# Kernel optimization log

Measured on AMD Instinct MI355X. Metric: run time of the kernel, lower is better.

The kernel has to match this reference:

```python
import jax, jax.numpy as jnp
import numpy as np

D_MODEL = 1024
N_HEADS = 16
D_HEAD = D_MODEL // N_HEADS
WINDOW = 256


def setup_inputs() -> dict:
    key = jax.random.key(0)
    ks = jax.random.split(key, 9)
    x = jax.random.normal(ks[0], (1, 4096, D_MODEL), dtype=jnp.float32)
    s = 0.02
    params = {
        'q_w': jax.random.normal(ks[1], (D_MODEL, D_MODEL), jnp.float32) * s,
        'q_b': jax.random.normal(ks[2], (D_MODEL,), jnp.float32) * s,
        'k_w': jax.random.normal(ks[3], (D_MODEL, D_MODEL), jnp.float32) * s,
        'k_b': jax.random.normal(ks[4], (D_MODEL,), jnp.float32) * s,
        'v_w': jax.random.normal(ks[5], (D_MODEL, D_MODEL), jnp.float32) * s,
        'v_b': jax.random.normal(ks[6], (D_MODEL,), jnp.float32) * s,
        'o_w': jax.random.normal(ks[7], (D_MODEL, D_MODEL), jnp.float32) * s,
        'o_b': jax.random.normal(ks[8], (D_MODEL,), jnp.float32) * s,
    }
    return {'x': x, **params}


def reference(x, q_w, q_b, k_w, k_b, v_w, v_b, o_w, o_b):
    B, S, D = x.shape
    scale = jnp.sqrt(jnp.float32(D_HEAD))
    # torch nn.Linear: y = x @ W.T + b
    q = (x @ q_w.T + q_b).reshape(B, S, N_HEADS, D_HEAD).transpose(0, 2, 1, 3)
    k = (x @ k_w.T + k_b).reshape(B, S, N_HEADS, D_HEAD).transpose(0, 2, 1, 3)
    v = (x @ v_w.T + v_b).reshape(B, S, N_HEADS, D_HEAD).transpose(0, 2, 1, 3)
    scores = jnp.einsum('bhqd,bhkd->bhqk', q, k) / scale  # [B,H,S,S]
    idx = jnp.arange(S)
    row = idx[:, None]
    col = idx[None, :]
    masked = (col > row) | (row - col >= min(WINDOW, S))
    scores = jnp.where(masked[None, None], -jnp.inf, scores)
    attn = jax.nn.softmax(scores, axis=-1)
    attn = jnp.nan_to_num(attn, nan=0.0)
    out = jnp.einsum('bhqk,bhkd->bhqd', attn, v)
    out = out.transpose(0, 2, 1, 3).reshape(B, S, D)
    return out @ o_w.T + o_b
```

## Files before the change

### kernel.cpp

```cpp
#include <hip/hip_runtime.h>

typedef __attribute__((ext_vector_type(4))) float f32x4;
typedef __attribute__((ext_vector_type(16))) float f32x16;
typedef __attribute__((ext_vector_type(8))) short short8;
typedef __attribute__((ext_vector_type(4))) int i32x4;

#define S_LEN 4096
#define DM    1024
#define NH    16
#define DH    64
#define WIN   256

__device__ inline unsigned short f2b(float f) {
  unsigned int x = __float_as_uint(f);
  unsigned int r = (x + 0x7fffu + ((x >> 16) & 1u)) >> 16;
  return (unsigned short)r;
}

__device__ inline void gload_lds16(const void* g, void* l) {
  __builtin_amdgcn_global_load_lds(
      (const __attribute__((address_space(1))) void*)g,
      (__attribute__((address_space(3))) void*)l, 16, 0, 0);
}

__global__ __launch_bounds__(256) void cvt_all(
    const float* __restrict__ x,
    const float* __restrict__ qw, const float* __restrict__ kw,
    const float* __restrict__ vw, const float* __restrict__ ow,
    unsigned short* __restrict__ Xb, unsigned short* __restrict__ Wb)
{
  const int y = blockIdx.y;
  const float* src;
  unsigned short* dst;
  int n8;
  if (y == 0) { src = x; dst = Xb; n8 = (S_LEN * DM) / 8; }
  else {
    src = (y == 1) ? qw : (y == 2) ? kw : (y == 3) ? vw : ow;
    dst = Wb + (size_t)(y - 1) * DM * DM;
    n8 = (DM * DM) / 8;
  }
  const int i = blockIdx.x * 256 + threadIdx.x;
  if (i >= n8) return;
  const float4* s4 = (const float4*)src + (size_t)i * 2;
  float4 a = s4[0], b = s4[1];
  short8 v;
  v[0] = f2b(a.x); v[1] = f2b(a.y); v[2] = f2b(a.z); v[3] = f2b(a.w);
  v[4] = f2b(b.x); v[5] = f2b(b.y); v[6] = f2b(b.z); v[7] = f2b(b.w);
  *(short8*)(dst + (size_t)i * 8) = v;
}

#define PIPE_WAIT8  asm volatile("s_waitcnt vmcnt(8)" ::: "memory")
#define PIPE_WAIT0  asm volatile("s_waitcnt vmcnt(0)" ::: "memory")
#define PIPE_BAR    do { __builtin_amdgcn_s_barrier(); __builtin_amdgcn_sched_barrier(0); } while (0)
#define PIPE_ENDBAR do { __builtin_amdgcn_sched_barrier(0); __builtin_amdgcn_s_barrier(); \
                         __builtin_amdgcn_sched_barrier(0); } while (0)

template<int BM, int BN, int NWM, int NWN, bool F32OUT>
__global__ __launch_bounds__(NWM* NWN * 64, 1) void gemm_bt(
    const unsigned short* __restrict__ A,
    const unsigned short* __restrict__ Wb,
    const float* __restrict__ b0, const float* __restrict__ b1, const float* __restrict__ b2,
    unsigned short* __restrict__ Obf,
    float* __restrict__ Of)
{
  constexpr int THREADS = NWM * NWN * 64;
  constexpr int MR = BM / (NWM * 16);
  constexpr int NR = BN / (NWN * 16);
  constexpr int RSM = BM / NWM;
  constexpr int RSN = BN / NWN;
  constexpr int REG = BM * 64;
  static_assert(BM == BN, "");
  static_assert((BM * 64 * 2) / (THREADS * 16) == 4, "4 staging rounds");

  const int z = blockIdx.z;
  const unsigned short* Bmat = Wb + (size_t)z * DM * DM;
  const float* bias = (z == 0) ? b0 : (z == 1) ? b1 : b2;
  unsigned short* O = Obf + (size_t)z * S_LEN * DM;

  __shared__ __align__(16) unsigned short LDS[4 * REG];
  unsigned short* A0 = LDS;
  unsigned short* A1 = LDS + REG;
  unsigned short* B0 = LDS + 2 * REG;
  unsigned short* B1 = LDS + 3 * REG;

  const int t = threadIdx.x;
  const int lane = t & 63, w = t >> 6;
  const int wm = w / NWN, wn = w % NWN;
  const int lr = lane & 15, lg = lane >> 4;
  const int m0 = blockIdx.x * BM, n0 = blockIdx.y * BN;

  int srow[4], scol[4], sbase[4];
#pragma unroll
  for (int i = 0; i < 4; ++i) {
    const int bo = (i * THREADS + w * 64) * 16;
    const int o = bo + lane * 16;
    const int row = o >> 7, colb = o & 127;
    const int colp = colb ^ ((row & 3) << 4) ^ (((row >> 2) & 1) << 6);
    srow[i] = row; scol[i] = colp >> 1; sbase[i] = bo >> 1;
  }

#define STAGE(e0, lA, lB)                                                           \
  do {                                                                              \
    _Pragma("unroll") for (int i = 0; i < 4; ++i) {                                 \
      gload_lds16(A + (size_t)(m0 + srow[i]) * DM + (e0) + scol[i], (lA) + sbase[i]); \
      gload_lds16(Bmat + (size_t)(n0 + srow[i]) * DM + (e0) + scol[i], (lB) + sbase[i]); \
    }                                                                               \
  } while (0)

  f32x4 acc[MR][NR];
#pragma unroll
  for (int m = 0; m < MR; ++m)
#pragma unroll
    for (int n = 0; n < NR; ++n) acc[m][n] = (f32x4){0.f, 0.f, 0.f, 0.f};

  const int xor6l = ((lr >> 2) & 1) << 6;
  const int xor45 = (lg << 4) ^ ((lr & 3) << 4);

#define COMPUTE(sAp, sBp)                                                           \
  do {                                                                              \
    _Pragma("unroll") for (int kk = 0; kk < 2; ++kk) {                              \
      const int coff = ((kk << 6) ^ xor6l) + xor45;                                 \
      short8 af[MR], bf[NR];                                                        \
      _Pragma("unroll") for (int m = 0; m < MR; ++m)                                \
        af[m] = *(const short8*)((const char*)(sAp) + (wm * RSM + m * 16 + lr) * 128 + coff); \
      _Pragma("unroll") for (int n = 0; n < NR; ++n)                                \
        bf[n] = *(const short8*)((const char*)(sBp) + (wn * RSN + n * 16 + lr) * 128 + coff); \
      _Pragma("unroll") for (int m = 0; m < MR; ++m)                                \
        _Pragma("unroll") for (int n = 0; n < NR; ++n)                              \
          acc[m][n] = __builtin_amdgcn_mfma_f32_16x16x32_bf16(af[m], bf[n], acc[m][n], 0, 0, 0); \
    }                                                                               \
  } while (0)

  STAGE(0, A0, B0);
#pragma unroll 1
  for (int kt = 0; kt < 14; kt += 2) {
    STAGE((kt + 1) * 64, A1, B1);
    PIPE_WAIT8; PIPE_BAR;
    __builtin_amdgcn_s_setprio(1);
    COMPUTE(A0, B0);
    __builtin_amdgcn_s_setprio(0);
    PIPE_ENDBAR;
    STAGE((kt + 2) * 64, A0, B0);
    PIPE_WAIT8; PIPE_BAR;
    __builtin_amdgcn_s_setprio(1);
    COMPUTE(A1, B1);
    __builtin_amdgcn_s_setprio(0);
    PIPE_ENDBAR;
  }
  STAGE(15 * 64, A1, B1);
  PIPE_WAIT8; PIPE_BAR;
  __builtin_amdgcn_s_setprio(1);
  COMPUTE(A0, B0);
  __builtin_amdgcn_s_setprio(0);
  PIPE_ENDBAR;
  PIPE_WAIT0; PIPE_BAR;
  __builtin_amdgcn_s_setprio(1);
  COMPUTE(A1, B1);
  __builtin_amdgcn_s_setprio(0);

#undef STAGE
#undef COMPUTE

#pragma unroll
  for (int n = 0; n < NR; ++n) {
    const int gc = n0 + wn * RSN + n * 16 + lr;
    const float bv = bias[gc];
#pragma unroll
    for (int m = 0; m < MR; ++m) {
      const int gr0 = m0 + wm * RSM + m * 16 + lg * 4;
#pragma unroll
      for (int r = 0; r < 4; ++r) {
        const float val = acc[m][n][r] + bv;
        if (F32OUT) Of[(size_t)(gr0 + r) * DM + gc] = val;
        else        O[(size_t)(gr0 + r) * DM + gc] = f2b(val);
      }
    }
  }
}

__global__ __launch_bounds__(256) void attn(
    const unsigned short* __restrict__ Q,
    const unsigned short* __restrict__ Km,
    const unsigned short* __restrict__ Vm,
    unsigned short* __restrict__ AO)
{
  const int warp = threadIdx.x >> 6;
  const int l = threadIdx.x & 63;
  const int qw0 = (blockIdx.x * 4 + warp) * 32;
  const int hD = blockIdx.y * DH;
  const int q = l & 31;
  const int hi = l >> 5;
  const int l31 = l & 31;
  const int vkey = (l & 15) * 2;
  const int vd0 = (l >> 4) * 16;

  __shared__ __align__(16) unsigned short VtS[4][2][64 * 40];
  unsigned short* vt0 = &VtS[warp][0][0];
  unsigned short* vt1 = &VtS[warp][1][0];

  short8 qf[4];
  {
    const unsigned short* qp = Q + (size_t)(qw0 + q) * DM + hD + hi * 8;
#pragma unroll
    for (int ks = 0; ks < 4; ++ks) qf[ks] = *(const short8*)(qp + ks * 16);
  }

  f32x16 o0{}, o1{};
  float lsum = 0.f;

  const int kb0 = (qw0 >= WIN) ? (qw0 - WIN) : 0;
  const int nch = (qw0 + 32 - kb0) >> 5;

  short8 kfA[4], vfA[4], kfB[4], vfB[4];

#define LOADKV(kb_, kf_, vf_)                                                    \
  do {                                                                           \
    const unsigned short* kp_ = Km + (size_t)((kb_) + l31) * DM + hD + hi * 8;   \
    (kf_)[0] = *(const short8*)kp_;                                              \
    (kf_)[1] = *(const short8*)(kp_ + 16);                                       \
    (kf_)[2] = *(const short8*)(kp_ + 32);                                       \
    (kf_)[3] = *(const short8*)(kp_ + 48);                                       \
    const unsigned short* vp_ = Vm + (size_t)((kb_) + vkey) * DM + hD + vd0;     \
    (vf_)[0] = *(const short8*)vp_;                                              \
    (vf_)[1] = *(const short8*)(vp_ + 8);                                        \
    (vf_)[2] = *(const short8*)(vp_ + DM);                                       \
    (vf_)[3] = *(const short8*)(vp_ + DM + 8);                                   \
  } while (0)

#define PROCESS(kb_, kf_, vf_, vt_)                                             \
  do {                                                                          \
    const int kbv = (kb_);                                                      \
    _Pragma("unroll") for (int j = 0; j < 16; ++j) {                            \
      unsigned int wv = (unsigned int)(unsigned short)(vf_)[j >> 3][j & 7]      \
          | ((unsigned int)(unsigned short)(vf_)[2 + (j >> 3)][j & 7] << 16);   \
      *(unsigned int*)((vt_) + (vd0 + j) * 40 + vkey) = wv;                     \
    }                                                                           \
    f32x16 s{};                                                                 \
    _Pragma("unroll") for (int ks = 0; ks < 4; ++ks)                            \
      s = __builtin_amdgcn_mfma_f32_32x32x16_bf16((kf_)[ks], qf[ks], s, 0, 0, 0); \
    float p[16];                                                                \
    const bool isEdge = (kbv >= qw0) || (kbv + WIN - 32 < qw0);                 \
    if (isEdge) {                                                               \
      _Pragma("unroll") for (int r = 0; r < 16; ++r) {                          \
        const int key = kbv + (r & 3) + 8 * (r >> 2) + 4 * hi;                  \
        const int qg = qw0 + q;                                                 \
        const bool valid = (key <= qg) && (qg - key < WIN);                     \
        p[r] = __expf(valid ? s[r] * 0.125f : -1e30f);                          \
        lsum += p[r];                                                           \
      }                                                                         \
    } else {                                                                    \
      _Pragma("unroll") for (int r = 0; r < 16; ++r) {                          \
        p[r] = __expf(s[r] * 0.125f);                                           \
        lsum += p[r];                                                           \
      }                                                                         \
    }                                                                           \
    unsigned int u[8];                                                          \
    _Pragma("unroll") for (int t2 = 0; t2 < 4; ++t2) {                          \
      u[2 * t2]     = (unsigned int)f2b(p[4 * t2])     | ((unsigned int)f2b(p[4 * t2 + 1]) << 16); \
      u[2 * t2 + 1] = (unsigned int)f2b(p[4 * t2 + 2]) | ((unsigned int)f2b(p[4 * t2 + 3]) << 16); \
    }                                                                           \
    const unsigned int sd0 = hi ? u[0] : u[2], sd1 = hi ? u[1] : u[3];          \
    const unsigned int rc0 = __shfl_xor(sd0, 32, 64), rc1 = __shfl_xor(sd1, 32, 64); \
    const unsigned int sd2 = hi ? u[4] : u[6], sd3 = hi ? u[5] : u[7];          \
    const unsigned int rc2 = __shfl_xor(sd2, 32, 64), rc3 = __shfl_xor(sd3, 32, 64); \
    i32x4 pw0, pw1;                                                             \
    pw0[0] = hi ? rc0 : u[0]; pw0[1] = hi ? rc1 : u[1];                         \
    pw0[2] = hi ? u[2] : rc0; pw0[3] = hi ? u[3] : rc1;                         \
    pw1[0] = hi ? rc2 : u[4]; pw1[1] = hi ? rc3 : u[5];                         \
    pw1[2] = hi ? u[6] : rc2; pw1[3] = hi ? u[7] : rc3;                         \
    const short8 pf0 = *(const short8*)&pw0;                                    \
    const short8 pf1 = *(const short8*)&pw1;                                    \
    const short8 a00 = *(const short8*)((vt_) + l31 * 40 + hi * 8);             \
    const short8 a01 = *(const short8*)((vt_) + l31 * 40 + 16 + hi * 8);        \
    const short8 a10 = *(const short8*)((vt_) + (32 + l31) * 40 + hi * 8);      \
    const short8 a11 = *(const short8*)((vt_) + (32 + l31) * 40 + 16 + hi * 8); \
    o0 = __builtin_amdgcn_mfma_f32_32x32x16_bf16(a00, pf0, o0, 0, 0, 0);        \
    o0 = __builtin_amdgcn_mfma_f32_32x32x16_bf16(a01, pf1, o0, 0, 0, 0);        \
    o1 = __builtin_amdgcn_mfma_f32_32x32x16_bf16(a10, pf0, o1, 0, 0, 0);        \
    o1 = __builtin_amdgcn_mfma_f32_32x32x16_bf16(a11, pf1, o1, 0, 0, 0);        \
  } while (0)

  LOADKV(kb0, kfA, vfA);
  int c = 0;
#pragma unroll 1
  for (; c + 2 <= nch; c += 2) {
    const int kb = kb0 + c * 32;
    LOADKV(kb + 32, kfB, vfB);
    PROCESS(kb, kfA, vfA, vt0);
    if (c + 2 < nch) LOADKV(kb + 64, kfA, vfA);
    PROCESS(kb + 32, kfB, vfB, vt1);
  }
  if (c < nch) PROCESS(kb0 + c * 32, kfA, vfA, vt0);

#undef LOADKV
#undef PROCESS

  lsum += __shfl_xor(lsum, 32, 64);
  const float inv = 1.f / lsum;
  unsigned short* aop = AO + (size_t)(qw0 + q) * DM + hD;
#pragma unroll
  for (int t2 = 0; t2 < 4; ++t2) {
    uint2 st;
    st.x = (unsigned int)f2b(o0[4 * t2] * inv)     | ((unsigned int)f2b(o0[4 * t2 + 1] * inv) << 16);
    st.y = (unsigned int)f2b(o0[4 * t2 + 2] * inv) | ((unsigned int)f2b(o0[4 * t2 + 3] * inv) << 16);
    *(uint2*)(aop + 8 * t2 + 4 * hi) = st;
    uint2 st2;
    st2.x = (unsigned int)f2b(o1[4 * t2] * inv)     | ((unsigned int)f2b(o1[4 * t2 + 1] * inv) << 16);
    st2.y = (unsigned int)f2b(o1[4 * t2 + 2] * inv) | ((unsigned int)f2b(o1[4 * t2 + 3] * inv) << 16);
    *(uint2*)(aop + 32 + 8 * t2 + 4 * hi) = st2;
  }
}

extern "C" void kernel_launch(void* const* d_in, const int* in_sizes, int n_in,
                              void* d_out, int out_size, void* d_ws, size_t ws_size,
                              hipStream_t stream) {
  const float* x  = (const float*)d_in[0];
  const float* qw = (const float*)d_in[1];
  const float* qb = (const float*)d_in[2];
  const float* kw = (const float*)d_in[3];
  const float* kb = (const float*)d_in[4];
  const float* vw = (const float*)d_in[5];
  const float* vb = (const float*)d_in[6];
  const float* ow = (const float*)d_in[7];
  const float* ob = (const float*)d_in[8];

  const size_t SD = (size_t)S_LEN * DM;
  unsigned short* Qb  = (unsigned short*)d_ws;
  unsigned short* Kb  = Qb + SD;
  unsigned short* Vb  = Kb + SD;
  unsigned short* AOb = Vb + SD;
  unsigned short* Xb  = AOb + SD;
  unsigned short* Wcv = Xb + SD;

  cvt_all<<<dim3(2048, 5), 256, 0, stream>>>(x, qw, kw, vw, ow, Xb, Wcv);
  gemm_bt<256, 256, 2, 4, false><<<dim3(16, 4, 3), 512, 0, stream>>>(
      Xb, Wcv, qb, kb, vb, Qb, nullptr);
  attn<<<dim3(S_LEN / 128, NH), 256, 0, stream>>>(Qb, Kb, Vb, AOb);
  gemm_bt<128, 128, 2, 2, true><<<dim3(32, 8, 1), 256, 0, stream>>>(
      AOb, Wcv + (size_t)3 * DM * DM, ob, ob, ob, nullptr, (float*)d_out);
}
```

Baseline: 86.64 us.

## Restructure QKV GEMM pipeline into 4-buffer K=32 stages without end barriers

Replaces the double-buffered K=64 staging with a four-buffer ring of K=32 tiles, prefetching two stages ahead and dropping the trailing barrier per iteration. The XOR-swizzled LDS layout is replaced by a plain row layout, and the launch bound no longer forces one block per CU. The aim is to hide global-to-LDS latency better and let more blocks share a CU. The unswizzled 64-byte rows may cause LDS bank conflicts, and smaller K steps add barrier overhead per unit of MFMA work.

```diff
diff --git a/kernel.cpp b/kernel.cpp
--- a/kernel.cpp
+++ b/kernel.cpp
@@ -49,14 +49,8 @@
   *(short8*)(dst + (size_t)i * 8) = v;
 }
 
-#define PIPE_WAIT8  asm volatile("s_waitcnt vmcnt(8)" ::: "memory")
-#define PIPE_WAIT0  asm volatile("s_waitcnt vmcnt(0)" ::: "memory")
-#define PIPE_BAR    do { __builtin_amdgcn_s_barrier(); __builtin_amdgcn_sched_barrier(0); } while (0)
-#define PIPE_ENDBAR do { __builtin_amdgcn_sched_barrier(0); __builtin_amdgcn_s_barrier(); \
-                         __builtin_amdgcn_sched_barrier(0); } while (0)
-
 template<int BM, int BN, int NWM, int NWN, bool F32OUT>
-__global__ __launch_bounds__(NWM* NWN * 64, 1) void gemm_bt(
+__global__ __launch_bounds__(NWM* NWN * 64) void gemm_bt(
     const unsigned short* __restrict__ A,
     const unsigned short* __restrict__ Wb,
     const float* __restrict__ b0, const float* __restrict__ b1, const float* __restrict__ b2,
@@ -68,20 +62,21 @@
   constexpr int NR = BN / (NWN * 16);
   constexpr int RSM = BM / NWM;
   constexpr int RSN = BN / NWN;
-  constexpr int REG = BM * 64;
-  static_assert(BM == BN, "");
-  static_assert((BM * 64 * 2) / (THREADS * 16) == 4, "4 staging rounds");
+  constexpr int ASZ = BM * 32;
+  constexpr int BUFSZ = ASZ + BN * 32;
+  static_assert((BM * 64) / (THREADS * 16) == 2, "2 A-loads per thread");
+  static_assert((BN * 64) / (THREADS * 16) == 2, "2 B-loads per thread");
 
   const int z = blockIdx.z;
   const unsigned short* Bmat = Wb + (size_t)z * DM * DM;
   const float* bias = (z == 0) ? b0 : (z == 1) ? b1 : b2;
   unsigned short* O = Obf + (size_t)z * S_LEN * DM;
 
-  __shared__ __align__(16) unsigned short LDS[4 * REG];
-  unsigned short* A0 = LDS;
-  unsigned short* A1 = LDS + REG;
-  unsigned short* B0 = LDS + 2 * REG;
-  unsigned short* B1 = LDS + 3 * REG;
+  __shared__ __align__(16) unsigned short LDS[4 * BUFSZ];
+  unsigned short* buf0 = LDS;
+  unsigned short* buf1 = LDS + BUFSZ;
+  unsigned short* buf2 = LDS + 2 * BUFSZ;
+  unsigned short* buf3 = LDS + 3 * BUFSZ;
 
   const int t = threadIdx.x;
   const int lane = t & 63, w = t >> 6;
@@ -89,22 +84,18 @@
   const int lr = lane & 15, lg = lane >> 4;
   const int m0 = blockIdx.x * BM, n0 = blockIdx.y * BN;
 
-  int srow[4], scol[4], sbase[4];
-#pragma unroll
-  for (int i = 0; i < 4; ++i) {
-    const int bo = (i * THREADS + w * 64) * 16;
-    const int o = bo + lane * 16;
-    const int row = o >> 7, colb = o & 127;
-    const int colp = colb ^ ((row & 3) << 4) ^ (((row >> 2) & 1) << 6);
-    srow[i] = row; scol[i] = colp >> 1; sbase[i] = bo >> 1;
-  }
-
-#define STAGE(e0, lA, lB)                                                           \
-  do {                                                                              \
-    _Pragma("unroll") for (int i = 0; i < 4; ++i) {                                 \
-      gload_lds16(A + (size_t)(m0 + srow[i]) * DM + (e0) + scol[i], (lA) + sbase[i]); \
-      gload_lds16(Bmat + (size_t)(n0 + srow[i]) * DM + (e0) + scol[i], (lB) + sbase[i]); \
-    }                                                                               \
+  const unsigned short* gA = A + (size_t)(m0 + (t >> 2)) * DM + (t & 3) * 8;
+  const unsigned short* gB = Bmat + (size_t)(n0 + (t >> 2)) * DM + (t & 3) * 8;
+  const int ldsOff = w * 64 * 8;
+
+#define STAGE(e0_, bufp_)                                                        \
+  do {                                                                           \
+    gload_lds16(gA + (e0_), (bufp_) + ldsOff);                                   \
+    gload_lds16(gA + (size_t)(THREADS / 4) * DM + (e0_),                         \
+                (bufp_) + THREADS * 8 + ldsOff);                                 \
+    gload_lds16(gB + (e0_), (bufp_) + ASZ + ldsOff);                             \
+    gload_lds16(gB + (size_t)(THREADS / 4) * DM + (e0_),                         \
+                (bufp_) + ASZ + THREADS * 8 + ldsOff);                           \
   } while (0)
 
   f32x4 acc[MR][NR];
@@ -113,53 +104,59 @@
 #pragma unroll
     for (int n = 0; n < NR; ++n) acc[m][n] = (f32x4){0.f, 0.f, 0.f, 0.f};
 
-  const int xor6l = ((lr >> 2) & 1) << 6;
-  const int xor45 = (lg << 4) ^ ((lr & 3) << 4);
-
-#define COMPUTE(sAp, sBp)                                                           \
-  do {                                                                              \
-    _Pragma("unroll") for (int kk = 0; kk < 2; ++kk) {                              \
-      const int coff = ((kk << 6) ^ xor6l) + xor45;                                 \
-      short8 af[MR], bf[NR];                                                        \
-      _Pragma("unroll") for (int m = 0; m < MR; ++m)                                \
-        af[m] = *(const short8*)((const char*)(sAp) + (wm * RSM + m * 16 + lr) * 128 + coff); \
-      _Pragma("unroll") for (int n = 0; n < NR; ++n)                                \
-        bf[n] = *(const short8*)((const char*)(sBp) + (wn * RSN + n * 16 + lr) * 128 + coff); \
-      _Pragma("unroll") for (int m = 0; m < MR; ++m)                                \
-        _Pragma("unroll") for (int n = 0; n < NR; ++n)                              \
-          acc[m][n] = __builtin_amdgcn_mfma_f32_16x16x32_bf16(af[m], bf[n], acc[m][n], 0, 0, 0); \
-    }                                                                               \
-  } while (0)
-
-  STAGE(0, A0, B0);
+#define COMPUTE(bufp_)                                                           \
+  do {                                                                           \
+    short8 af[MR], bf[NR];                                                       \
+    _Pragma("unroll") for (int m = 0; m < MR; ++m)                               \
+      af[m] = *(const short8*)((bufp_) + (wm * RSM + m * 16 + lr) * 32 + lg * 8); \
+    _Pragma("unroll") for (int n = 0; n < NR; ++n)                               \
+      bf[n] = *(const short8*)((bufp_) + ASZ + (wn * RSN + n * 16 + lr) * 32 + lg * 8); \
+    _Pragma("unroll") for (int m = 0; m < MR; ++m)                               \
+      _Pragma("unroll") for (int n = 0; n < NR; ++n)                             \
+        acc[m][n] = __builtin_amdgcn_mfma_f32_16x16x32_bf16(af[m], bf[n], acc[m][n], 0, 0, 0); \
+  } while (0)
+
+#define ITER(tt_, bufc_, bufs_)                                                  \
+  do {                                                                           \
+    STAGE(((tt_) + 2) * 32, bufs_);                                              \
+    asm volatile("s_waitcnt vmcnt(8)" ::: "memory");                             \
+    __builtin_amdgcn_s_barrier();                                                \
+    __builtin_amdgcn_sched_barrier(0);                                           \
+    __builtin_amdgcn_s_setprio(1);                                               \
+    COMPUTE(bufc_);                                                              \
+    __builtin_amdgcn_s_setprio(0);                                               \
+    __builtin_amdgcn_sched_barrier(0);                                           \
+  } while (0)
+
+#define ITER_TAIL(vm_, bufc_)                                                    \
+  do {                                                                           \
+    asm volatile("s_waitcnt vmcnt(" #vm_ ")" ::: "memory");                      \
+    __builtin_amdgcn_s_barrier();                                                \
+    __builtin_amdgcn_sched_barrier(0);                                           \
+    __builtin_amdgcn_s_setprio(1);                                               \
+    COMPUTE(bufc_);                                                              \
+    __builtin_amdgcn_s_setprio(0);                                               \
+    __builtin_amdgcn_sched_barrier(0);                                           \
+  } while (0)
+
+  STAGE(0, buf0);
+  STAGE(32, buf1);
 #pragma unroll 1
-  for (int kt = 0; kt < 14; kt += 2) {
-    STAGE((kt + 1) * 64, A1, B1);
-    PIPE_WAIT8; PIPE_BAR;
-    __builtin_amdgcn_s_setprio(1);
-    COMPUTE(A0, B0);
-    __builtin_amdgcn_s_setprio(0);
-    PIPE_ENDBAR;
-    STAGE((kt + 2) * 64, A0, B0);
-    PIPE_WAIT8; PIPE_BAR;
-    __builtin_amdgcn_s_setprio(1);
-    COMPUTE(A1, B1);
-    __builtin_amdgcn_s_setprio(0);
-    PIPE_ENDBAR;
-  }
-  STAGE(15 * 64, A1, B1);
-  PIPE_WAIT8; PIPE_BAR;
-  __builtin_amdgcn_s_setprio(1);
-  COMPUTE(A0, B0);
-  __builtin_amdgcn_s_setprio(0);
-  PIPE_ENDBAR;
-  PIPE_WAIT0; PIPE_BAR;
-  __builtin_amdgcn_s_setprio(1);
-  COMPUTE(A1, B1);
-  __builtin_amdgcn_s_setprio(0);
+  for (int tb = 0; tb < 28; tb += 4) {
+    ITER(tb + 0, buf0, buf2);
+    ITER(tb + 1, buf1, buf3);
+    ITER(tb + 2, buf2, buf0);
+    ITER(tb + 3, buf3, buf1);
+  }
+  ITER(28, buf0, buf2);
+  ITER(29, buf1, buf3);
+  ITER_TAIL(4, buf2);
+  ITER_TAIL(0, buf3);
 
 #undef STAGE
 #undef COMPUTE
+#undef ITER
+#undef ITER_TAIL
 
 #pragma unroll
   for (int n = 0; n < NR; ++n) {
```

Result: no change. 87.37 us (+0.8%).

## Split attention key range across two warps per query tile and combine via LDS

Applied to the files above, without the earlier changes.

Each 32-query tile is now handled by two warps, each processing half of the key chunks. The partial outputs and row sums are combined through shared memory. The grid doubles in x to give more waves and a shorter per-warp serial chain in the attention kernel, at the cost of two block barriers and an LDS reduction. It also skips exp on masked entries, switches the bf16 packing to the HIP intrinsic, and sets a min-blocks launch bound.

```diff
diff --git a/kernel.cpp b/kernel.cpp
--- a/kernel.cpp
+++ b/kernel.cpp
@@ -1,4 +1,5 @@
 #include <hip/hip_runtime.h>
+#include <hip/hip_bf16.h>
 
 typedef __attribute__((ext_vector_type(4))) float f32x4;
 typedef __attribute__((ext_vector_type(16))) float f32x16;
@@ -178,7 +179,7 @@
   }
 }
 
-__global__ __launch_bounds__(256) void attn(
+__global__ __launch_bounds__(256, 4) void attn(
     const unsigned short* __restrict__ Q,
     const unsigned short* __restrict__ Km,
     const unsigned short* __restrict__ Vm,
@@ -186,7 +187,9 @@
 {
   const int warp = threadIdx.x >> 6;
   const int l = threadIdx.x & 63;
-  const int qw0 = (blockIdx.x * 4 + warp) * 32;
+  const int qt = warp >> 1;
+  const int half = warp & 1;
+  const int qw0 = (blockIdx.x * 2 + qt) * 32;
   const int hD = blockIdx.y * DH;
   const int q = l & 31;
   const int hi = l >> 5;
@@ -194,9 +197,11 @@
   const int vkey = (l & 15) * 2;
   const int vd0 = (l >> 4) * 16;
 
-  __shared__ __align__(16) unsigned short VtS[4][2][64 * 40];
-  unsigned short* vt0 = &VtS[warp][0][0];
-  unsigned short* vt1 = &VtS[warp][1][0];
+  __shared__ __align__(16) char SMEM[40960];
+  unsigned short* vt0 = (unsigned short*)SMEM + warp * 2 * 2560;
+  unsigned short* vt1 = vt0 + 2560;
+  float* comb = (float*)SMEM;
+  float* clsum = (float*)(SMEM + 2 * 64 * 36 * 4);
 
   short8 qf[4];
   {
@@ -210,6 +215,9 @@
 
   const int kb0 = (qw0 >= WIN) ? (qw0 - WIN) : 0;
   const int nch = (qw0 + 32 - kb0) >> 5;
+  const int nlo = nch >> 1;
+  const int myn = half ? (nch - nlo) : nlo;
+  const int kbh = kb0 + (half ? nlo : 0) * 32;
 
   short8 kfA[4], vfA[4], kfB[4], vfB[4];
 
@@ -245,7 +253,7 @@
         const int key = kbv + (r & 3) + 8 * (r >> 2) + 4 * hi;                  \
         const int qg = qw0 + q;                                                 \
         const bool valid = (key <= qg) && (qg - key < WIN);                     \
-        p[r] = __expf(valid ? s[r] * 0.125f : -1e30f);                          \
+        p[r] = valid ? __expf(s[r] * 0.125f) : 0.f;                             \
         lsum += p[r];                                                           \
       }                                                                         \
     } else {                                                                    \
@@ -256,8 +264,10 @@
     }                                                                           \
     unsigned int u[8];                                                          \
     _Pragma("unroll") for (int t2 = 0; t2 < 4; ++t2) {                          \
-      u[2 * t2]     = (unsigned int)f2b(p[4 * t2])     | ((unsigned int)f2b(p[4 * t2 + 1]) << 16); \
-      u[2 * t2 + 1] = (unsigned int)f2b(p[4 * t2 + 2]) | ((unsigned int)f2b(p[4 * t2 + 3]) << 16); \
+      __hip_bfloat162 h0_ = __float22bfloat162_rn(make_float2(p[4 * t2], p[4 * t2 + 1])); \
+      __hip_bfloat162 h1_ = __float22bfloat162_rn(make_float2(p[4 * t2 + 2], p[4 * t2 + 3])); \
+      u[2 * t2]     = *(unsigned int*)&h0_;                                     \
+      u[2 * t2 + 1] = *(unsigned int*)&h1_;                                     \
     }                                                                           \
     const unsigned int sd0 = hi ? u[0] : u[2], sd1 = hi ? u[1] : u[3];          \
     const unsigned int rc0 = __shfl_xor(sd0, 32, 64), rc1 = __shfl_xor(sd1, 32, 64); \
@@ -280,34 +290,56 @@
     o1 = __builtin_amdgcn_mfma_f32_32x32x16_bf16(a11, pf1, o1, 0, 0, 0);        \
   } while (0)
 
-  LOADKV(kb0, kfA, vfA);
+  LOADKV(kbh, kfA, vfA);
   int c = 0;
 #pragma unroll 1
-  for (; c + 2 <= nch; c += 2) {
-    const int kb = kb0 + c * 32;
+  for (; c + 2 <= myn; c += 2) {
+    const int kb = kbh + c * 32;
     LOADKV(kb + 32, kfB, vfB);
     PROCESS(kb, kfA, vfA, vt0);
-    if (c + 2 < nch) LOADKV(kb + 64, kfA, vfA);
+    if (c + 2 < myn) LOADKV(kb + 64, kfA, vfA);
     PROCESS(kb + 32, kfB, vfB, vt1);
   }
-  if (c < nch) PROCESS(kb0 + c * 32, kfA, vfA, vt0);
+  if (c < myn) PROCESS(kbh + c * 32, kfA, vfA, vt0);
 
 #undef LOADKV
 #undef PROCESS
 
-  lsum += __shfl_xor(lsum, 32, 64);
-  const float inv = 1.f / lsum;
-  unsigned short* aop = AO + (size_t)(qw0 + q) * DM + hD;
-#pragma unroll
-  for (int t2 = 0; t2 < 4; ++t2) {
-    uint2 st;
-    st.x = (unsigned int)f2b(o0[4 * t2] * inv)     | ((unsigned int)f2b(o0[4 * t2 + 1] * inv) << 16);
-    st.y = (unsigned int)f2b(o0[4 * t2 + 2] * inv) | ((unsigned int)f2b(o0[4 * t2 + 3] * inv) << 16);
-    *(uint2*)(aop + 8 * t2 + 4 * hi) = st;
-    uint2 st2;
-    st2.x = (unsigned int)f2b(o1[4 * t2] * inv)     | ((unsigned int)f2b(o1[4 * t2 + 1] * inv) << 16);
-    st2.y = (unsigned int)f2b(o1[4 * t2 + 2] * inv) | ((unsigned int)f2b(o1[4 * t2 + 3] * inv) << 16);
-    *(uint2*)(aop + 32 + 8 * t2 + 4 * hi) = st2;
+  __syncthreads();
+  if (half == 0) {
+    float* cb = comb + (qt * 64 + l) * 36;
+#pragma unroll
+    for (int t2 = 0; t2 < 4; ++t2) {
+      *(f32x4*)(cb + t2 * 4)      = (f32x4){o0[4*t2], o0[4*t2+1], o0[4*t2+2], o0[4*t2+3]};
+      *(f32x4*)(cb + 16 + t2 * 4) = (f32x4){o1[4*t2], o1[4*t2+1], o1[4*t2+2], o1[4*t2+3]};
+    }
+    clsum[qt * 64 + l] = lsum;
+  }
+  __syncthreads();
+  if (half == 1) {
+    const float* cb = comb + (qt * 64 + l) * 36;
+#pragma unroll
+    for (int t2 = 0; t2 < 4; ++t2) {
+      f32x4 pa = *(const f32x4*)(cb + t2 * 4);
+      f32x4 pb = *(const f32x4*)(cb + 16 + t2 * 4);
+#pragma unroll
+      for (int j = 0; j < 4; ++j) { o0[4*t2+j] += pa[j]; o1[4*t2+j] += pb[j]; }
+    }
+    lsum += clsum[qt * 64 + l];
+    lsum += __shfl_xor(lsum, 32, 64);
+    const float inv = 1.f / lsum;
+    unsigned short* aop = AO + (size_t)(qw0 + q) * DM + hD;
+#pragma unroll
+    for (int t2 = 0; t2 < 4; ++t2) {
+      __hip_bfloat162 s0 = __float22bfloat162_rn(make_float2(o0[4*t2] * inv, o0[4*t2+1] * inv));
+      __hip_bfloat162 s1 = __float22bfloat162_rn(make_float2(o0[4*t2+2] * inv, o0[4*t2+3] * inv));
+      uint2 st; st.x = *(unsigned int*)&s0; st.y = *(unsigned int*)&s1;
+      *(uint2*)(aop + 8 * t2 + 4 * hi) = st;
+      __hip_bfloat162 s2 = __float22bfloat162_rn(make_float2(o1[4*t2] * inv, o1[4*t2+1] * inv));
+      __hip_bfloat162 s3 = __float22bfloat162_rn(make_float2(o1[4*t2+2] * inv, o1[4*t2+3] * inv));
+      uint2 st2; st2.x = *(unsigned int*)&s2; st2.y = *(unsigned int*)&s3;
+      *(uint2*)(aop + 32 + 8 * t2 + 4 * hi) = st2;
+    }
   }
 }
 
@@ -335,7 +367,7 @@
   cvt_all<<<dim3(2048, 5), 256, 0, stream>>>(x, qw, kw, vw, ow, Xb, Wcv);
   gemm_bt<256, 256, 2, 4, false><<<dim3(16, 4, 3), 512, 0, stream>>>(
       Xb, Wcv, qb, kb, vb, Qb, nullptr);
-  attn<<<dim3(S_LEN / 128, NH), 256, 0, stream>>>(Qb, Kb, Vb, AOb);
+  attn<<<dim3(S_LEN / 64, NH), 256, 0, stream>>>(Qb, Kb, Vb, AOb);
   gemm_bt<128, 128, 2, 2, true><<<dim3(32, 8, 1), 256, 0, stream>>>(
       AOb, Wcv + (size_t)3 * DM * DM, ob, ob, ob, nullptr, (float*)d_out);
 }
```

Measured after the change: 123.8 us. +42.9%, slower.

## Fuse QKV projection into one N=3072 GEMM with 256x192 tiles

Applied to the files above, without the earlier changes.

The three Q/K/V projections become a single GEMM over the concatenated 3072-wide weight matrix. It uses 256x192 tiles and a 16x16 grid, giving 256 blocks instead of 192, to fill more of the CU array. The epilogue routes each output column to the right Q/K/V buffer and bias. Attention masking now skips the exp for invalid keys, and bf16 packing switches to the library paired conversion. Risks are uneven tile shapes (3 B staging rounds against 4 A rounds, adjusted by the vmcnt(7) waits) and register pressure from the 8x3 accumulator.

```diff
diff --git a/kernel.cpp b/kernel.cpp
--- a/kernel.cpp
+++ b/kernel.cpp
@@ -1,4 +1,5 @@
 #include <hip/hip_runtime.h>
+#include <hip/hip_bf16.h>
 
 typedef __attribute__((ext_vector_type(4))) float f32x4;
 typedef __attribute__((ext_vector_type(16))) float f32x16;
@@ -50,33 +51,129 @@
 }
 
 #define PIPE_WAIT8  asm volatile("s_waitcnt vmcnt(8)" ::: "memory")
+#define PIPE_WAIT7  asm volatile("s_waitcnt vmcnt(7)" ::: "memory")
 #define PIPE_WAIT0  asm volatile("s_waitcnt vmcnt(0)" ::: "memory")
 #define PIPE_BAR    do { __builtin_amdgcn_s_barrier(); __builtin_amdgcn_sched_barrier(0); } while (0)
 #define PIPE_ENDBAR do { __builtin_amdgcn_sched_barrier(0); __builtin_amdgcn_s_barrier(); \
                          __builtin_amdgcn_sched_barrier(0); } while (0)
 
-template<int BM, int BN, int NWM, int NWN, bool F32OUT>
-__global__ __launch_bounds__(NWM* NWN * 64, 1) void gemm_bt(
+__global__ __launch_bounds__(512, 1) void gemm_qkv_fused(
     const unsigned short* __restrict__ A,
-    const unsigned short* __restrict__ Wb,
-    const float* __restrict__ b0, const float* __restrict__ b1, const float* __restrict__ b2,
-    unsigned short* __restrict__ Obf,
+    const unsigned short* __restrict__ W,
+    const float* __restrict__ bq, const float* __restrict__ bk, const float* __restrict__ bv,
+    unsigned short* __restrict__ Qb)
+{
+  constexpr int BM = 256, BN = 192;
+  constexpr int REGA = BM * 64;
+  constexpr int BUF = REGA + BN * 64;
+  __shared__ __align__(16) unsigned short LDS[2 * BUF];
+  unsigned short* A0 = LDS;
+  unsigned short* B0 = LDS + REGA;
+  unsigned short* A1 = LDS + BUF;
+  unsigned short* B1 = LDS + BUF + REGA;
+
+  const int t = threadIdx.x;
+  const int lane = t & 63, w = t >> 6;
+  const int wm = w >> 2, wn = w & 3;
+  const int lr = lane & 15, lg = lane >> 4;
+  const int m0 = blockIdx.x * BM, n0 = blockIdx.y * BN;
+
+  int sr[4], sc[4], sb[4];
+#pragma unroll
+  for (int i = 0; i < 4; ++i) {
+    const int bo = (i * 512 + w * 64) * 16;
+    const int o = bo + lane * 16;
+    const int row = o >> 7, colb = o & 127;
+    const int colp = colb ^ ((row & 3) << 4) ^ (((row >> 2) & 1) << 6);
+    sr[i] = row; sc[i] = colp >> 1; sb[i] = bo >> 1;
+  }
+
+#define STAGE(e0, lA, lB)                                                           \
+  do {                                                                              \
+    _Pragma("unroll") for (int i = 0; i < 4; ++i)                                   \
+      gload_lds16(A + (size_t)(m0 + sr[i]) * DM + (e0) + sc[i], (lA) + sb[i]);      \
+    _Pragma("unroll") for (int i = 0; i < 3; ++i)                                   \
+      gload_lds16(W + (size_t)(n0 + sr[i]) * DM + (e0) + sc[i], (lB) + sb[i]);      \
+  } while (0)
+
+  f32x4 acc[8][3];
+#pragma unroll
+  for (int m = 0; m < 8; ++m)
+#pragma unroll
+    for (int n = 0; n < 3; ++n) acc[m][n] = (f32x4){0.f, 0.f, 0.f, 0.f};
+
+  const int xor6l = ((lr >> 2) & 1) << 6;
+  const int xor45 = (lg << 4) ^ ((lr & 3) << 4);
+
+#define COMPUTE(sAp, sBp)                                                           \
+  do {                                                                              \
+    _Pragma("unroll") for (int kk = 0; kk < 2; ++kk) {                              \
+      const int coff = ((kk << 6) ^ xor6l) + xor45;                                 \
+      short8 af[8], bf[3];                                                          \
+      _Pragma("unroll") for (int m = 0; m < 8; ++m)                                 \
+        af[m] = *(const short8*)((const char*)(sAp) + (wm * 128 + m * 16 + lr) * 128 + coff); \
+      _Pragma("unroll") for (int n = 0; n < 3; ++n)                                 \
+        bf[n] = *(const short8*)((const char*)(sBp) + (wn * 48 + n * 16 + lr) * 128 + coff); \
+      _Pragma("unroll") for (int m = 0; m < 8; ++m)                                 \
+        _Pragma("unroll") for (int n = 0; n < 3; ++n)                               \
+          acc[m][n] = __builtin_amdgcn_mfma_f32_16x16x32_bf16(af[m], bf[n], acc[m][n], 0, 0, 0); \
+    }                                                                               \
+  } while (0)
+
+  STAGE(0, A0, B0);
+#pragma unroll 1
+  for (int kt = 0; kt < 14; kt += 2) {
+    STAGE((kt + 1) * 64, A1, B1);
+    PIPE_WAIT7; PIPE_BAR;
+    __builtin_amdgcn_s_setprio(1);
+    COMPUTE(A0, B0);
+    __builtin_amdgcn_s_setprio(0);
+    PIPE_ENDBAR;
+    STAGE((kt + 2) * 64, A0, B0);
+    PIPE_WAIT7; PIPE_BAR;
+    __builtin_amdgcn_s_setprio(1);
+    COMPUTE(A1, B1);
+    __builtin_amdgcn_s_setprio(0);
+    PIPE_ENDBAR;
+  }
+  STAGE(15 * 64, A1, B1);
+  PIPE_WAIT7; PIPE_BAR;
+  __builtin_amdgcn_s_setprio(1);
+  COMPUTE(A0, B0);
+  __builtin_amdgcn_s_setprio(0);
+  PIPE_ENDBAR;
+  PIPE_WAIT0; PIPE_BAR;
+  __builtin_amdgcn_s_setprio(1);
+  COMPUTE(A1, B1);
+  __builtin_amdgcn_s_setprio(0);
+
+#undef STAGE
+#undef COMPUTE
+
+#pragma unroll
+  for (int n = 0; n < 3; ++n) {
+    const int gc = n0 + wn * 48 + n * 16 + lr;
+    const int slice = gc >> 10, col = gc & 1023;
+    const float* bp = (slice == 0) ? bq : (slice == 1) ? bk : bv;
+    const float bv_ = bp[col];
+    unsigned short* Obase = Qb + (size_t)slice * ((size_t)S_LEN * DM);
+#pragma unroll
+    for (int m = 0; m < 8; ++m) {
+      const int gr0 = m0 + wm * 128 + m * 16 + lg * 4;
+#pragma unroll
+      for (int r = 0; r < 4; ++r)
+        Obase[(size_t)(gr0 + r) * DM + col] = f2b(acc[m][n][r] + bv_);
+    }
+  }
+}
+
+__global__ __launch_bounds__(256, 1) void gemm_out(
+    const unsigned short* __restrict__ A,
+    const unsigned short* __restrict__ Bmat,
+    const float* __restrict__ bias,
     float* __restrict__ Of)
 {
-  constexpr int THREADS = NWM * NWN * 64;
-  constexpr int MR = BM / (NWM * 16);
-  constexpr int NR = BN / (NWN * 16);
-  constexpr int RSM = BM / NWM;
-  constexpr int RSN = BN / NWN;
-  constexpr int REG = BM * 64;
-  static_assert(BM == BN, "");
-  static_assert((BM * 64 * 2) / (THREADS * 16) == 4, "4 staging rounds");
-
-  const int z = blockIdx.z;
-  const unsigned short* Bmat = Wb + (size_t)z * DM * DM;
-  const float* bias = (z == 0) ? b0 : (z == 1) ? b1 : b2;
-  unsigned short* O = Obf + (size_t)z * S_LEN * DM;
-
+  constexpr int REG = 128 * 64;
   __shared__ __align__(16) unsigned short LDS[4 * REG];
   unsigned short* A0 = LDS;
   unsigned short* A1 = LDS + REG;
@@ -85,33 +182,33 @@
 
   const int t = threadIdx.x;
   const int lane = t & 63, w = t >> 6;
-  const int wm = w / NWN, wn = w % NWN;
+  const int wm = w >> 1, wn = w & 1;
   const int lr = lane & 15, lg = lane >> 4;
-  const int m0 = blockIdx.x * BM, n0 = blockIdx.y * BN;
-
-  int srow[4], scol[4], sbase[4];
+  const int m0 = blockIdx.x * 128, n0 = blockIdx.y * 128;
+
+  int sr[4], sc[4], sb[4];
 #pragma unroll
   for (int i = 0; i < 4; ++i) {
-    const int bo = (i * THREADS + w * 64) * 16;
+    const int bo = (i * 256 + w * 64) * 16;
     const int o = bo + lane * 16;
     const int row = o >> 7, colb = o & 127;
     const int colp = colb ^ ((row & 3) << 4) ^ (((row >> 2) & 1) << 6);
-    srow[i] = row; scol[i] = colp >> 1; sbase[i] = bo >> 1;
+    sr[i] = row; sc[i] = colp >> 1; sb[i] = bo >> 1;
   }
 
 #define STAGE(e0, lA, lB)                                                           \
   do {                                                                              \
     _Pragma("unroll") for (int i = 0; i < 4; ++i) {                                 \
-      gload_lds16(A + (size_t)(m0 + srow[i]) * DM + (e0) + scol[i], (lA) + sbase[i]); \
-      gload_lds16(Bmat + (size_t)(n0 + srow[i]) * DM + (e0) + scol[i], (lB) + sbase[i]); \
+      gload_lds16(A + (size_t)(m0 + sr[i]) * DM + (e0) + sc[i], (lA) + sb[i]);      \
+      gload_lds16(Bmat + (size_t)(n0 + sr[i]) * DM + (e0) + sc[i], (lB) + sb[i]);   \
     }                                                                               \
   } while (0)
 
-  f32x4 acc[MR][NR];
-#pragma unroll
-  for (int m = 0; m < MR; ++m)
-#pragma unroll
-    for (int n = 0; n < NR; ++n) acc[m][n] = (f32x4){0.f, 0.f, 0.f, 0.f};
+  f32x4 acc[4][4];
+#pragma unroll
+  for (int m = 0; m < 4; ++m)
+#pragma unroll
+    for (int n = 0; n < 4; ++n) acc[m][n] = (f32x4){0.f, 0.f, 0.f, 0.f};
 
   const int xor6l = ((lr >> 2) & 1) << 6;
   const int xor45 = (lg << 4) ^ ((lr & 3) << 4);
@@ -120,13 +217,13 @@
   do {                                                                              \
     _Pragma("unroll") for (int kk = 0; kk < 2; ++kk) {                              \
       const int coff = ((kk << 6) ^ xor6l) + xor45;                                 \
-      short8 af[MR], bf[NR];                                                        \
-      _Pragma("unroll") for (int m = 0; m < MR; ++m)                                \
-        af[m] = *(const short8*)((const char*)(sAp) + (wm * RSM + m * 16 + lr) * 128 + coff); \
-      _Pragma("unroll") for (int n = 0; n < NR; ++n)                                \
-        bf[n] = *(const short8*)((const char*)(sBp) + (wn * RSN + n * 16 + lr) * 128 + coff); \
-      _Pragma("unroll") for (int m = 0; m < MR; ++m)                                \
-        _Pragma("unroll") for (int n = 0; n < NR; ++n)                              \
+      short8 af[4], bf[4];                                                          \
+      _Pragma("unroll") for (int m = 0; m < 4; ++m)                                 \
+        af[m] = *(const short8*)((const char*)(sAp) + (wm * 64 + m * 16 + lr) * 128 + coff); \
+      _Pragma("unroll") for (int n = 0; n < 4; ++n)                                 \
+        bf[n] = *(const short8*)((const char*)(sBp) + (wn * 64 + n * 16 + lr) * 128 + coff); \
+      _Pragma("unroll") for (int m = 0; m < 4; ++m)                                 \
+        _Pragma("unroll") for (int n = 0; n < 4; ++n)                               \
           acc[m][n] = __builtin_amdgcn_mfma_f32_16x16x32_bf16(af[m], bf[n], acc[m][n], 0, 0, 0); \
     }                                                                               \
   } while (0)
@@ -162,18 +259,15 @@
 #undef COMPUTE
 
 #pragma unroll
-  for (int n = 0; n < NR; ++n) {
-    const int gc = n0 + wn * RSN + n * 16 + lr;
+  for (int n = 0; n < 4; ++n) {
+    const int gc = n0 + wn * 64 + n * 16 + lr;
     const float bv = bias[gc];
 #pragma unroll
-    for (int m = 0; m < MR; ++m) {
-      const int gr0 = m0 + wm * RSM + m * 16 + lg * 4;
-#pragma unroll
-      for (int r = 0; r < 4; ++r) {
-        const float val = acc[m][n][r] + bv;
-        if (F32OUT) Of[(size_t)(gr0 + r) * DM + gc] = val;
-        else        O[(size_t)(gr0 + r) * DM + gc] = f2b(val);
-      }
+    for (int m = 0; m < 4; ++m) {
+      const int gr0 = m0 + wm * 64 + m * 16 + lg * 4;
+#pragma unroll
+      for (int r = 0; r < 4; ++r)
+        Of[(size_t)(gr0 + r) * DM + gc] = acc[m][n][r] + bv;
     }
   }
 }
@@ -245,7 +339,7 @@
         const int key = kbv + (r & 3) + 8 * (r >> 2) + 4 * hi;                  \
         const int qg = qw0 + q;                                                 \
         const bool valid = (key <= qg) && (qg - key < WIN);                     \
-        p[r] = __expf(valid ? s[r] * 0.125f : -1e30f);                          \
+        p[r] = valid ? __expf(s[r] * 0.125f) : 0.f;                             \
         lsum += p[r];                                                           \
       }                                                                         \
     } else {                                                                    \
@@ -256,8 +350,10 @@
     }                                                                           \
     unsigned int u[8];                                                          \
     _Pragma("unroll") for (int t2 = 0; t2 < 4; ++t2) {                          \
-      u[2 * t2]     = (unsigned int)f2b(p[4 * t2])     | ((unsigned int)f2b(p[4 * t2 + 1]) << 16); \
-      u[2 * t2 + 1] = (unsigned int)f2b(p[4 * t2 + 2]) | ((unsigned int)f2b(p[4 * t2 + 3]) << 16); \
+      __hip_bfloat162 h0_ = __float22bfloat162_rn(make_float2(p[4 * t2], p[4 * t2 + 1])); \
+      __hip_bfloat162 h1_ = __float22bfloat162_rn(make_float2(p[4 * t2 + 2], p[4 * t2 + 3])); \
+      u[2 * t2]     = *(unsigned int*)&h0_;                                     \
+      u[2 * t2 + 1] = *(unsigned int*)&h1_;                                     \
     }                                                                           \
     const unsigned int sd0 = hi ? u[0] : u[2], sd1 = hi ? u[1] : u[3];          \
     const unsigned int rc0 = __shfl_xor(sd0, 32, 64), rc1 = __shfl_xor(sd1, 32, 64); \
@@ -300,13 +396,13 @@
   unsigned short* aop = AO + (size_t)(qw0 + q) * DM + hD;
 #pragma unroll
   for (int t2 = 0; t2 < 4; ++t2) {
-    uint2 st;
-    st.x = (unsigned int)f2b(o0[4 * t2] * inv)     | ((unsigned int)f2b(o0[4 * t2 + 1] * inv) << 16);
-    st.y = (unsigned int)f2b(o0[4 * t2 + 2] * inv) | ((unsigned int)f2b(o0[4 * t2 + 3] * inv) << 16);
+    __hip_bfloat162 s0 = __float22bfloat162_rn(make_float2(o0[4*t2] * inv, o0[4*t2+1] * inv));
+    __hip_bfloat162 s1 = __float22bfloat162_rn(make_float2(o0[4*t2+2] * inv, o0[4*t2+3] * inv));
+    uint2 st; st.x = *(unsigned int*)&s0; st.y = *(unsigned int*)&s1;
     *(uint2*)(aop + 8 * t2 + 4 * hi) = st;
-    uint2 st2;
-    st2.x = (unsigned int)f2b(o1[4 * t2] * inv)     | ((unsigned int)f2b(o1[4 * t2 + 1] * inv) << 16);
-    st2.y = (unsigned int)f2b(o1[4 * t2 + 2] * inv) | ((unsigned int)f2b(o1[4 * t2 + 3] * inv) << 16);
+    __hip_bfloat162 s2 = __float22bfloat162_rn(make_float2(o1[4*t2] * inv, o1[4*t2+1] * inv));
+    __hip_bfloat162 s3 = __float22bfloat162_rn(make_float2(o1[4*t2+2] * inv, o1[4*t2+3] * inv));
+    uint2 st2; st2.x = *(unsigned int*)&s2; st2.y = *(unsigned int*)&s3;
     *(uint2*)(aop + 32 + 8 * t2 + 4 * hi) = st2;
   }
 }
@@ -333,9 +429,7 @@
   unsigned short* Wcv = Xb + SD;
 
   cvt_all<<<dim3(2048, 5), 256, 0, stream>>>(x, qw, kw, vw, ow, Xb, Wcv);
-  gemm_bt<256, 256, 2, 4, false><<<dim3(16, 4, 3), 512, 0, stream>>>(
-      Xb, Wcv, qb, kb, vb, Qb, nullptr);
+  gemm_qkv_fused<<<dim3(16, 16), 512, 0, stream>>>(Xb, Wcv, qb, kb, vb, Qb);
   attn<<<dim3(S_LEN / 128, NH), 256, 0, stream>>>(Qb, Kb, Vb, AOb);
-  gemm_bt<128, 128, 2, 2, true><<<dim3(32, 8, 1), 256, 0, stream>>>(
-      AOb, Wcv + (size_t)3 * DM * DM, ob, ob, ob, nullptr, (float*)d_out);
-}
+  gemm_out<<<dim3(32, 8), 256, 0, stream>>>(AOb, Wcv + (size_t)3 * DM * DM, ob, (float*)d_out);
+}
```

Result: faster. 81.58 us (median of 2 runs) (-5.8%).
